# Optimization experiments

Measured on AMD Instinct MI355X. Metric: run time of the kernel, lower is better.

The kernel has to match this reference:

```python
import jax, jax.numpy as jnp
import numpy as np

N_NODES = 100000
N_EDGES = 1600000
DIM = 128


def setup_inputs() -> dict:
    key = jax.random.key(0)
    k1, k2, k3, k4 = jax.random.split(key, 4)
    x = jax.random.normal(k1, (N_NODES, DIM), dtype=jnp.float32)
    edge_index = jax.random.randint(k2, (2, N_EDGES), 0, N_NODES, dtype=jnp.int64)
    # PyG GCNConv params: Linear weight [out, in] (glorot) and bias [out] (zeros -> use small randn for a non-trivial grad path)
    W = jax.random.normal(k3, (DIM, DIM), dtype=jnp.float32) * (1.0 / np.sqrt(DIM))
    b = jax.random.normal(k4, (DIM,), dtype=jnp.float32) * 0.01
    return {"x": x, "edge_index": edge_index, "W": W, "b": b}


def reference(x, edge_index, W, b):
    # Faithful GCNConv: add self-loops, symmetric deg^-1/2 normalization,
    # linear transform, scatter-add aggregation, bias.
    N = x.shape[0]
    loop = jnp.arange(N, dtype=edge_index.dtype)
    src = jnp.concatenate([edge_index[0], loop])  # [E+N]
    dst = jnp.concatenate([edge_index[1], loop])  # [E+N]

    # degree (with self-loops) on destination nodes
    deg = jax.ops.segment_sum(jnp.ones_like(dst, dtype=x.dtype), dst, num_segments=N)
    dinv = jnp.where(deg > 0, jax.lax.rsqrt(deg), 0.0)
    norm = dinv[src] * dinv[dst]  # [E+N]

    x_lin = x @ W.T  # [N, dim] — PyG applies linear before propagate
    msg = x_lin[src] * norm[:, None]  # [E+N, dim] gather + scale
    out = jax.ops.segment_sum(msg, dst, num_segments=N)  # scatter-add aggregate
    return out + b
```

## Files before the change

kernel.cpp:

```cpp
#include <hip/hip_runtime.h>
#include <hip/hip_bf16.h>


#define DIM 128
#define BINSHIFT 9
#define BINSZ 512
#define NB 196
#define MAXNB 256
#define CAPB 16384
#define WSTRIDE 136
#define SCAT_BLOCKS 256

typedef __attribute__((ext_vector_type(8))) short short8;
typedef __attribute__((ext_vector_type(4))) float f32x4;
typedef __attribute__((ext_vector_type(4))) unsigned short ushort4v;

__device__ inline unsigned short f2bf(float f) {
    unsigned u = __builtin_bit_cast(unsigned, f);
    return (unsigned short)((u + 0x7FFFu + ((u >> 16) & 1u)) >> 16);
}

__device__ inline void bf8_axpy(uint4 v, float s, float* acc) {
    acc[0] = fmaf(s, __builtin_bit_cast(float, v.x << 16), acc[0]);
    acc[1] = fmaf(s, __builtin_bit_cast(float, v.x & 0xFFFF0000u), acc[1]);
    acc[2] = fmaf(s, __builtin_bit_cast(float, v.y << 16), acc[2]);
    acc[3] = fmaf(s, __builtin_bit_cast(float, v.y & 0xFFFF0000u), acc[3]);
    acc[4] = fmaf(s, __builtin_bit_cast(float, v.z << 16), acc[4]);
    acc[5] = fmaf(s, __builtin_bit_cast(float, v.z & 0xFFFF0000u), acc[5]);
    acc[6] = fmaf(s, __builtin_bit_cast(float, v.w << 16), acc[6]);
    acc[7] = fmaf(s, __builtin_bit_cast(float, v.w & 0xFFFF0000u), acc[7]);
}

__global__ __launch_bounds__(256) void wconv(const float* __restrict__ W,
                                             unsigned short* __restrict__ wbf) {
    int base = blockIdx.x * 1024 + threadIdx.x * 4;
#pragma unroll
    for (int i = 0; i < 4; ++i) {
        float4 w4 = ((const float4*)W)[base + i];
        ushort4v o; o.x = f2bf(w4.x); o.y = f2bf(w4.y); o.z = f2bf(w4.z); o.w = f2bf(w4.w);
        ((ushort4v*)wbf)[base + i] = o;
    }
}

__global__ __launch_bounds__(256) void scatter_gemm(const int* __restrict__ ei, int E,
                                                    int* __restrict__ binCursor,
                                                    int2* __restrict__ binned,
                                                    const float* __restrict__ x,
                                                    const unsigned short* __restrict__ wbf,
                                                    unsigned short* __restrict__ xlin, int N) {
    __shared__ __align__(16) char smem[4 * 16 * WSTRIDE * 2];
    int t = threadIdx.x;

    if (blockIdx.x < SCAT_BLOCKS) {
        int* lh = (int*)smem;
        int* lbase = lh + MAXNB;
        lh[t] = 0;
        __syncthreads();
        int chunk = (E + SCAT_BLOCKS - 1) / SCAT_BLOCKS;
        int base = blockIdx.x * chunk, end = min(E, base + chunk);
        for (int i = base + t; i < end; i += 256)
            atomicAdd(&lh[ei[E + i] >> BINSHIFT], 1);
        __syncthreads();
        if (t < NB) {
            int c = lh[t];
            lbase[t] = c ? atomicAdd(&binCursor[t], c) : 0;
            lh[t] = 0;
        }
        __syncthreads();
        for (int i = base + t; i < end; i += 256) {
            int s = ei[i], d = ei[E + i];
            int b = d >> BINSHIFT;
            int pos = b * CAPB + lbase[b] + atomicAdd(&lh[b], 1);
            binned[pos] = make_int2(s, d);
        }
        return;
    }

    unsigned short* obuf = (unsigned short*)smem;
    int wid = t >> 6, lane = t & 63;
    int m = lane & 15, quad = lane >> 4;
    int row_base = (blockIdx.x - SCAT_BLOCKS) * 64 + wid * 16;

    f32x4 acc[8];
#pragma unroll
    for (int j = 0; j < 8; ++j) acc[j] = (f32x4){0.f, 0.f, 0.f, 0.f};

    int arow = row_base + m;
    if (arow >= N) arow = N - 1;
    const float* xr = x + (size_t)arow * DIM + quad * 8;

#pragma unroll
    for (int kc = 0; kc < 4; ++kc) {
        float4 a0 = *(const float4*)(xr + kc * 32);
        float4 a1 = *(const float4*)(xr + kc * 32 + 4);
        short8 af;
        af[0] = (short)f2bf(a0.x); af[1] = (short)f2bf(a0.y);
        af[2] = (short)f2bf(a0.z); af[3] = (short)f2bf(a0.w);
        af[4] = (short)f2bf(a1.x); af[5] = (short)f2bf(a1.y);
        af[6] = (short)f2bf(a1.z); af[7] = (short)f2bf(a1.w);
#pragma unroll
        for (int jt = 0; jt < 8; ++jt) {
            short8 bf = *(const short8*)&wbf[(jt * 16 + m) * DIM + kc * 32 + quad * 8];
            acc[jt] = __builtin_amdgcn_mfma_f32_16x16x32_bf16(af, bf, acc[jt], 0, 0, 0);
        }
    }

    unsigned short* ob = &obuf[wid * 16 * WSTRIDE];
#pragma unroll
    for (int jt = 0; jt < 8; ++jt)
#pragma unroll
        for (int r = 0; r < 4; ++r)
            ob[(quad * 4 + r) * WSTRIDE + jt * 16 + m] = f2bf(acc[jt][r]);
    __syncthreads();
#pragma unroll
    for (int it = 0; it < 4; ++it) {
        int idx = it * 64 + lane;
        int r = idx >> 4;
        int cb = idx & 15;
        int grow = row_base + r;
        if (grow < N) {
            short8 v = *(const short8*)&ob[r * WSTRIDE + cb * 8];
            *(short8*)(xlin + (size_t)grow * DIM + cb * 8) = v;
        }
    }
}

__global__ __launch_bounds__(512) void csr_build(const int2* __restrict__ binned,
                                                 const int* __restrict__ binCursor,
                                                 int* __restrict__ col,
                                                 int2* __restrict__ rowinfo,
                                                 float* __restrict__ dinv, int N) {
    __shared__ int ldeg[BINSZ], sa[BINSZ], sb[BINSZ], lcur[BINSZ];
    int t = threadIdx.x;
    int b = blockIdx.x;
    int s0 = b * CAPB;
    int s1 = s0 + binCursor[b];

    ldeg[t] = 0; lcur[t] = 0;
    __syncthreads();
    for (int i = s0 + t; i < s1; i += 512)
        atomicAdd(&ldeg[binned[i].y & (BINSZ - 1)], 1);
    __syncthreads();
    sa[t] = ldeg[t];
    __syncthreads();
    int* src = sa; int* dstp = sb;
    for (int step = 1; step < BINSZ; step <<= 1) {
        int v = src[t];
        if (t >= step) v += src[t - step];
        dstp[t] = v;
        __syncthreads();
        int* tmp = src; src = dstp; dstp = tmp;
    }
    int d = ldeg[t];
    int startoff = src[t] - d;
    int n = (b << BINSHIFT) + t;
    if (n < N) {
        rowinfo[n] = make_int2(s0 + startoff, d);
        dinv[n] = rsqrtf((float)(d + 1));
    }
    dstp[t] = startoff;
    __syncthreads();
    for (int i = s0 + t; i < s1; i += 512) {
        int2 e = binned[i];
        int li = e.y & (BINSZ - 1);
        col[s0 + dstp[li] + atomicAdd(&lcur[li], 1)] = e.x;
    }
}


__global__ __launch_bounds__(256) void aggregate(const unsigned short* __restrict__ xlin,
                                                 const int* __restrict__ col,
                                                 const int2* __restrict__ rowinfo,
                                                 const float* __restrict__ dinv,
                                                 const float* __restrict__ bias,
                                                 float* __restrict__ out, int N) {
    int node = blockIdx.x * 16 + (threadIdx.x >> 4);
    int lane = threadIdx.x & 15;
    if (node >= N) return;

    float di = dinv[node];
    int2 ri = rowinfo[node];
    int r0 = ri.x, r1 = ri.x + ri.y;

    const uint4* xl = (const uint4*)xlin;
    float acc[8] = {};
    bf8_axpy(xl[(size_t)node * 16 + lane], di, acc);

    for (int i = r0; i < r1; i += 4) {
        int rem = r1 - i;
        int s0 = col[i];
        int s1 = col[rem > 1 ? i + 1 : i];
        int s2 = col[rem > 2 ? i + 2 : i];
        int s3 = col[rem > 3 ? i + 3 : i];
        float d0 = dinv[s0];
        float d1 = rem > 1 ? dinv[s1] : 0.f;
        float d2 = rem > 2 ? dinv[s2] : 0.f;
        float d3 = rem > 3 ? dinv[s3] : 0.f;
        uint4 v0 = xl[(size_t)s0 * 16 + lane];
        uint4 v1 = xl[(size_t)s1 * 16 + lane];
        uint4 v2 = xl[(size_t)s2 * 16 + lane];
        uint4 v3 = xl[(size_t)s3 * 16 + lane];
        bf8_axpy(v0, d0, acc);
        bf8_axpy(v1, d1, acc);
        bf8_axpy(v2, d2, acc);
        bf8_axpy(v3, d3, acc);
    }

    const float4* b4 = (const float4*)(bias + lane * 8);
    float4 bl = b4[0], bh = b4[1];
    float4 olo = make_float4(di * acc[0] + bl.x, di * acc[1] + bl.y,
                             di * acc[2] + bl.z, di * acc[3] + bl.w);
    float4 ohi = make_float4(di * acc[4] + bh.x, di * acc[5] + bh.y,
                             di * acc[6] + bh.z, di * acc[7] + bh.w);
    float4* op = (float4*)(out + (size_t)node * DIM + lane * 8);
    op[0] = olo;
    op[1] = ohi;
}


extern "C" void kernel_launch(void* const* d_in, const int* in_sizes, int n_in,
                              void* d_out, int out_size, void* d_ws, size_t ws_size,
                              hipStream_t stream) {
    const float* x    = (const float*)d_in[0];
    const int*   ei   = (const int*)d_in[1];
    const float* W    = (const float*)d_in[2];
    const float* bias = (const float*)d_in[3];
    float* out = (float*)d_out;

    const int N = in_sizes[0] / DIM;
    const int E = in_sizes[1] / 2;

    char* ws = (char*)d_ws;
    size_t off = 0;
    auto alloc = [&](size_t bytes) { size_t o = off; off = (off + bytes + 255) & ~(size_t)255; return o; };
    unsigned short* xlin = (unsigned short*)(ws + alloc((size_t)N * DIM * 2));
    int2* binned   = (int2*) (ws + alloc((size_t)NB * CAPB * 8));
    int*  col      = (int*)  (ws + alloc((size_t)NB * CAPB * 4));
    int2* rowinfo  = (int2*) (ws + alloc((size_t)N * 8));
    float* dinv    = (float*)(ws + alloc((size_t)N * 4));
    int*  binCursor= (int*)  (ws + alloc(MAXNB * 4));
    unsigned short* wbf = (unsigned short*)(ws + alloc((size_t)DIM * DIM * 2));

    int GB = (N + 63) / 64;

    hipMemsetAsync(binCursor, 0, MAXNB * 4, stream);
    wconv<<<4, 256, 0, stream>>>(W, wbf);
    scatter_gemm<<<SCAT_BLOCKS + GB, 256, 0, stream>>>(ei, E, binCursor, binned, x, wbf, xlin, N);
    csr_build<<<NB, 512, 0, stream>>>(binned, binCursor, col, rowinfo, dinv, N);
    aggregate<<<(N + 15) / 16, 256, 0, stream>>>(xlin, col, rowinfo, dinv, bias, out, N);
}
```

Baseline: 229.5 us.

## Pack edges into 32-bit words, buffer bin scatter in LDS, fuse CSR build with GEMM

The edge binning now packs each edge's local destination and source into one 32-bit word, halving binned traffic. It uses 256-node bins and stages edges in per-bin LDS buffers, flushing them in 16-element vector chunks to get coalesced global writes. The W conversion is folded into the scatter kernel, and the CSR build is fused with the GEMM so they overlap in one launch, which removes two launches. Risks include the 17-bit source packing limit (which holds for N=100000), overflow of the LDS buffer onto a slower per-edge global atomic path, and fewer scatter blocks (128) reducing parallelism.

```diff
diff --git a/kernel.cpp b/kernel.cpp
--- a/kernel.cpp
+++ b/kernel.cpp
@@ -3,13 +3,14 @@
 
 
 #define DIM 128
-#define BINSHIFT 9
-#define BINSZ 512
-#define NB 196
-#define MAXNB 256
-#define CAPB 16384
+#define BINSHIFT 8
+#define BINSZ 256
+#define NB 391
+#define CAPB 8192
+#define BUFCAP 40
+#define SBLK 128
+#define ROUND 2048
 #define WSTRIDE 136
-#define SCAT_BLOCKS 256
 
 typedef __attribute__((ext_vector_type(8))) short short8;
 typedef __attribute__((ext_vector_type(4))) float f32x4;
@@ -31,47 +32,129 @@
     acc[7] = fmaf(s, __builtin_bit_cast(float, v.w & 0xFFFF0000u), acc[7]);
 }
 
-__global__ __launch_bounds__(256) void wconv(const float* __restrict__ W,
-                                             unsigned short* __restrict__ wbf) {
-    int base = blockIdx.x * 1024 + threadIdx.x * 4;
-#pragma unroll
-    for (int i = 0; i < 4; ++i) {
-        float4 w4 = ((const float4*)W)[base + i];
-        ushort4v o; o.x = f2bf(w4.x); o.y = f2bf(w4.y); o.z = f2bf(w4.z); o.w = f2bf(w4.w);
-        ((ushort4v*)wbf)[base + i] = o;
-    }
-}
-
-__global__ __launch_bounds__(256) void scatter_gemm(const int* __restrict__ ei, int E,
-                                                    int* __restrict__ binCursor,
-                                                    int2* __restrict__ binned,
-                                                    const float* __restrict__ x,
-                                                    const unsigned short* __restrict__ wbf,
-                                                    unsigned short* __restrict__ xlin, int N) {
-    __shared__ __align__(16) char smem[4 * 16 * WSTRIDE * 2];
+__global__ __launch_bounds__(512) void scatter_ms(const int* __restrict__ ei, int E,
+                                                  int* __restrict__ binCursor,
+                                                  unsigned* __restrict__ binned,
+                                                  const float* __restrict__ W,
+                                                  unsigned short* __restrict__ wbf) {
     int t = threadIdx.x;
-
-    if (blockIdx.x < SCAT_BLOCKS) {
-        int* lh = (int*)smem;
-        int* lbase = lh + MAXNB;
-        lh[t] = 0;
-        __syncthreads();
-        int chunk = (E + SCAT_BLOCKS - 1) / SCAT_BLOCKS;
-        int base = blockIdx.x * chunk, end = min(E, base + chunk);
-        for (int i = base + t; i < end; i += 256)
-            atomicAdd(&lh[ei[E + i] >> BINSHIFT], 1);
-        __syncthreads();
-        if (t < NB) {
-            int c = lh[t];
-            lbase[t] = c ? atomicAdd(&binCursor[t], c) : 0;
-            lh[t] = 0;
-        }
-        __syncthreads();
-        for (int i = base + t; i < end; i += 256) {
-            int s = ei[i], d = ei[E + i];
+    if ((int)blockIdx.x >= SBLK) {
+        int base = ((int)blockIdx.x - SBLK) * 2048 + t * 4;
+#pragma unroll
+        for (int i = 0; i < 4; ++i) {
+            float4 w4 = ((const float4*)W)[base + i];
+            ushort4v o; o.x = f2bf(w4.x); o.y = f2bf(w4.y); o.z = f2bf(w4.z); o.w = f2bf(w4.w);
+            ((ushort4v*)wbf)[base + i] = o;
+        }
+        return;
+    }
+
+    __shared__ int cnt[NB];
+    __shared__ unsigned buf[NB * BUFCAP];
+    for (int i = t; i < NB; i += 512) cnt[i] = 0;
+    __syncthreads();
+
+    int chunk = (E + SBLK - 1) / SBLK;
+    int base = blockIdx.x * chunk;
+    int end = min(E, base + chunk);
+
+    for (int rb = base; rb < end; rb += ROUND) {
+        int re = min(end, rb + ROUND);
+        for (int i = rb + t; i < re; i += 512) {
+            int s = ei[i];
+            int d = ei[E + i];
             int b = d >> BINSHIFT;
-            int pos = b * CAPB + lbase[b] + atomicAdd(&lh[b], 1);
-            binned[pos] = make_int2(s, d);
+            unsigned p = ((unsigned)(d & (BINSZ - 1)) << 17) | (unsigned)s;
+            int pos = atomicAdd(&cnt[b], 1);
+            if (pos < BUFCAP) buf[b * BUFCAP + pos] = p;
+            else binned[(size_t)b * CAPB + atomicAdd(&binCursor[b], 1)] = p;
+        }
+        __syncthreads();
+        for (int b = t; b < NB; b += 512) {
+            int c = min(cnt[b], BUFCAP);
+            int full = c & ~15;
+            if (full > 0) {
+                int gbase = atomicAdd(&binCursor[b], full);
+                unsigned* gp = binned + (size_t)b * CAPB + gbase;
+                const unsigned* lp = &buf[b * BUFCAP];
+                if ((gbase & 3) == 0) {
+                    for (int g = 0; g < full; g += 4)
+                        *(uint4*)(gp + g) = *(const uint4*)(lp + g);
+                } else {
+                    for (int g = 0; g < full; ++g) gp[g] = lp[g];
+                }
+                int rem = c - full;
+                for (int j = 0; j < rem; ++j)
+                    buf[b * BUFCAP + j] = buf[b * BUFCAP + full + j];
+                cnt[b] = rem;
+            } else {
+                cnt[b] = c;
+            }
+        }
+        __syncthreads();
+    }
+    for (int b = t; b < NB; b += 512) {
+        int c = min(cnt[b], BUFCAP);
+        if (c > 0) {
+            int gbase = atomicAdd(&binCursor[b], c);
+            unsigned* gp = binned + (size_t)b * CAPB + gbase;
+            for (int j = 0; j < c; ++j) gp[j] = buf[b * BUFCAP + j];
+        }
+    }
+}
+
+__global__ __launch_bounds__(512) void csr_gemm(const unsigned* __restrict__ binned,
+                                                const int* __restrict__ binCursor,
+                                                int* __restrict__ col,
+                                                int2* __restrict__ rowinfo,
+                                                float* __restrict__ dinv,
+                                                const float* __restrict__ x,
+                                                const unsigned short* __restrict__ wbf,
+                                                unsigned short* __restrict__ xlin, int N) {
+    __shared__ __align__(16) char smem[8 * 16 * WSTRIDE * 2];
+    int t = threadIdx.x;
+
+    if ((int)blockIdx.x < NB) {
+        int* ldeg = (int*)smem;
+        int* sa   = ldeg + BINSZ;
+        int* sb2  = sa + BINSZ;
+        int* lcur = sb2 + BINSZ;
+        int b = blockIdx.x;
+        int s0 = b * CAPB;
+        int s1 = s0 + binCursor[b];
+
+        if (t < BINSZ) { ldeg[t] = 0; lcur[t] = 0; }
+        __syncthreads();
+        for (int i = s0 + t; i < s1; i += 512)
+            atomicAdd(&ldeg[binned[i] >> 17], 1);
+        __syncthreads();
+        if (t < BINSZ) sa[t] = ldeg[t];
+        __syncthreads();
+        int* src = sa; int* dstp = sb2;
+        for (int step = 1; step < BINSZ; step <<= 1) {
+            if (t < BINSZ) {
+                int v = src[t];
+                if (t >= step) v += src[t - step];
+                dstp[t] = v;
+            }
+            __syncthreads();
+            int* tmp = src; src = dstp; dstp = tmp;
+        }
+        if (t < BINSZ) {
+            int d = ldeg[t];
+            int startoff = src[t] - d;
+            int n = (b << BINSHIFT) + t;
+            if (n < N) {
+                rowinfo[n] = make_int2(s0 + startoff, d);
+                dinv[n] = rsqrtf((float)(d + 1));
+            }
+            dstp[t] = startoff;
+        }
+        __syncthreads();
+        for (int i = s0 + t; i < s1; i += 512) {
+            unsigned p = binned[i];
+            int li = p >> 17;
+            col[s0 + dstp[li] + atomicAdd(&lcur[li], 1)] = (int)(p & 0x1FFFFu);
         }
         return;
     }
@@ -79,7 +162,7 @@
     unsigned short* obuf = (unsigned short*)smem;
     int wid = t >> 6, lane = t & 63;
     int m = lane & 15, quad = lane >> 4;
-    int row_base = (blockIdx.x - SCAT_BLOCKS) * 64 + wid * 16;
+    int row_base = ((int)blockIdx.x - NB) * 128 + wid * 16;
 
     f32x4 acc[8];
 #pragma unroll
@@ -122,48 +205,6 @@
             short8 v = *(const short8*)&ob[r * WSTRIDE + cb * 8];
             *(short8*)(xlin + (size_t)grow * DIM + cb * 8) = v;
         }
-    }
-}
-
-__global__ __launch_bounds__(512) void csr_build(const int2* __restrict__ binned,
-                                                 const int* __restrict__ binCursor,
-                                                 int* __restrict__ col,
-                                                 int2* __restrict__ rowinfo,
-                                                 float* __restrict__ dinv, int N) {
-    __shared__ int ldeg[BINSZ], sa[BINSZ], sb[BINSZ], lcur[BINSZ];
-    int t = threadIdx.x;
-    int b = blockIdx.x;
-    int s0 = b * CAPB;
-    int s1 = s0 + binCursor[b];
-
-    ldeg[t] = 0; lcur[t] = 0;
-    __syncthreads();
-    for (int i = s0 + t; i < s1; i += 512)
-        atomicAdd(&ldeg[binned[i].y & (BINSZ - 1)], 1);
-    __syncthreads();
-    sa[t] = ldeg[t];
-    __syncthreads();
-    int* src = sa; int* dstp = sb;
-    for (int step = 1; step < BINSZ; step <<= 1) {
-        int v = src[t];
-        if (t >= step) v += src[t - step];
-        dstp[t] = v;
-        __syncthreads();
-        int* tmp = src; src = dstp; dstp = tmp;
-    }
-    int d = ldeg[t];
-    int startoff = src[t] - d;
-    int n = (b << BINSHIFT) + t;
-    if (n < N) {
-        rowinfo[n] = make_int2(s0 + startoff, d);
-        dinv[n] = rsqrtf((float)(d + 1));
-    }
-    dstp[t] = startoff;
-    __syncthreads();
-    for (int i = s0 + t; i < s1; i += 512) {
-        int2 e = binned[i];
-        int li = e.y & (BINSZ - 1);
-        col[s0 + dstp[li] + atomicAdd(&lcur[li], 1)] = e.x;
     }
 }
 
@@ -234,18 +275,17 @@
     size_t off = 0;
     auto alloc = [&](size_t bytes) { size_t o = off; off = (off + bytes + 255) & ~(size_t)255; return o; };
     unsigned short* xlin = (unsigned short*)(ws + alloc((size_t)N * DIM * 2));
-    int2* binned   = (int2*) (ws + alloc((size_t)NB * CAPB * 8));
+    unsigned* binned = (unsigned*)(ws + alloc((size_t)NB * CAPB * 4));
     int*  col      = (int*)  (ws + alloc((size_t)NB * CAPB * 4));
     int2* rowinfo  = (int2*) (ws + alloc((size_t)N * 8));
     float* dinv    = (float*)(ws + alloc((size_t)N * 4));
-    int*  binCursor= (int*)  (ws + alloc(MAXNB * 4));
+    int*  binCursor= (int*)  (ws + alloc((size_t)NB * 4 + 256));
     unsigned short* wbf = (unsigned short*)(ws + alloc((size_t)DIM * DIM * 2));
 
-    int GB = (N + 63) / 64;
-
-    hipMemsetAsync(binCursor, 0, MAXNB * 4, stream);
-    wconv<<<4, 256, 0, stream>>>(W, wbf);
-    scatter_gemm<<<SCAT_BLOCKS + GB, 256, 0, stream>>>(ei, E, binCursor, binned, x, wbf, xlin, N);
-    csr_build<<<NB, 512, 0, stream>>>(binned, binCursor, col, rowinfo, dinv, N);
+    int GB = (N + 127) / 128;
+
+    hipMemsetAsync(binCursor, 0, (size_t)NB * 4, stream);
+    scatter_ms<<<SBLK + 2, 512, 0, stream>>>(ei, E, binCursor, binned, W, wbf);
+    csr_gemm<<<NB + GB, 512, 0, stream>>>(binned, binCursor, col, rowinfo, dinv, x, wbf, xlin, N);
     aggregate<<<(N + 15) / 16, 256, 0, stream>>>(xlin, col, rowinfo, dinv, bias, out, N);
 }
```

New measurement: 232.3 us. About the same (+1.2%).
